# Kernel tuning notes

Measured on AMD Instinct MI355X. Metric: run time of the kernel, lower is better.

The kernel has to match this reference:

```python
import jax, jax.numpy as jnp
import numpy as np

D = 1024      # input_dim == memory_dim
HID = 1024    # hid_dim
NEG = 1e30


def setup_inputs() -> dict:
    key = jax.random.key(0)
    ks = jax.random.split(key, 9)
    N, LD, LM = 8, 2048, 512
    s = 1.0 / np.sqrt(D)
    return {
        "input": jax.random.normal(ks[0], (N, LD, D), jnp.float32),
        "memory": jax.random.normal(ks[1], (N, LM, D), jnp.float32),
        "mask": jnp.ones((N, LM), jnp.float32),
        # input_linear_1 / memory_linear_1: Linear(d, 1, bias=False)
        "in1_w": jax.random.normal(ks[2], (D,), jnp.float32) * s,
        "mem1_w": jax.random.normal(ks[3], (D,), jnp.float32) * s,
        # input_linear_2 / memory_linear_2: Linear(d, hid, bias=True), stored [d, hid]
        "in2_w": jax.random.normal(ks[4], (D, HID), jnp.float32) * s,
        "in2_b": jax.random.normal(ks[5], (HID,), jnp.float32) * s,
        "mem2_w": jax.random.normal(ks[6], (D, HID), jnp.float32) * s,
        "mem2_b": jax.random.normal(ks[7], (HID,), jnp.float32) * s,
    }


def reference(input, memory, mask, in1_w, mem1_w, in2_w, in2_b, mem2_w, mem2_b):
    # dropout=0.0 / eval mode -> identity
    dot_scale = jnp.asarray(np.sqrt(D), input.dtype)
    input_dot = jnp.einsum("nld,d->nl", input, in1_w)[:, :, None]      # [N,Ld,1]
    memory_dot = jnp.einsum("nmd,d->nm", memory, mem1_w)[:, None, :]   # [N,1,Lm]
    cross_dot = jnp.einsum("nld,nmd->nlm", input, memory) / dot_scale  # [N,Ld,Lm]
    att = input_dot + memory_dot + cross_dot
    att = att - NEG * (1.0 - mask[:, None, :])

    inp2 = jnp.einsum("nld,dh->nlh", input, in2_w) + in2_b    # [N,Ld,hid]
    mem2 = jnp.einsum("nmd,dh->nmh", memory, mem2_w) + mem2_b  # [N,Lm,hid]

    weight_one = jax.nn.softmax(att, axis=-1)                 # [N,Ld,Lm]
    output_one = jnp.einsum("nlm,nmh->nlh", weight_one, mem2)  # [N,Ld,hid]

    weight_two = jax.nn.softmax(jnp.max(att, axis=-1), axis=-1)  # [N,Ld]
    output_two = jnp.einsum("nl,nlh->nh", weight_two, inp2)[:, None, :]  # [N,1,hid]

    out = jnp.concatenate(
        [inp2, output_one, inp2 * output_one, output_two * output_one], axis=-1
    )  # [N,Ld,4*hid]
    return out, mem2
```

## Files before the change

kernel.cpp:

```cpp
#include <hip/hip_runtime.h>

typedef unsigned short u16;
typedef __attribute__((ext_vector_type(8))) short short8;
typedef __attribute__((ext_vector_type(4))) float f32x4;
typedef __attribute__((ext_vector_type(4))) unsigned short u16x4;

#define NSEQ 8
#define LD 2048
#define LM 512
#define DD 1024
#define HID 1024
#define M1 (NSEQ*LD)
#define M2 (NSEQ*LM)

#define GLOAD_LDS16(gp, lp) __builtin_amdgcn_global_load_lds( \
    (const __attribute__((address_space(1))) unsigned int*)(gp), \
    (__attribute__((address_space(3))) unsigned int*)(lp), 16, 0, 0)

__device__ __forceinline__ u16 f2bf(float f) {
    union { float f; unsigned int i; } v; v.f = f;
    unsigned int r = v.i + 0x7fffu + ((v.i >> 16) & 1u);
    return (u16)(r >> 16);
}
__device__ __forceinline__ float bf2f(u16 u) {
    union { unsigned int i; float f; } v; v.i = ((unsigned int)u) << 16; return v.f;
}

__global__ __launch_bounds__(256) void prep_rows2(
    const float* __restrict__ input, const float* __restrict__ memory,
    const float* __restrict__ in1_w, const float* __restrict__ mem1_w,
    const float* __restrict__ mask,
    u16* __restrict__ input_bf16, u16* __restrict__ memory_bf16,
    float* __restrict__ idot, float* __restrict__ mdotm) {
    const int row = blockIdx.x, t = threadIdx.x;
    const float* src; const float* w; u16* dst;
    if (row < M1) { src = input + (size_t)row * DD; w = in1_w;
                    dst = input_bf16 + (size_t)row * DD; }
    else { const int rm = row - M1; src = memory + (size_t)rm * DD; w = mem1_w;
           dst = memory_bf16 + (size_t)rm * DD; }
    f32x4 v = *(const f32x4*)(src + t * 4);
    f32x4 wv = *(const f32x4*)(w + t * 4);
    u16x4 o;
    #pragma unroll
    for (int i = 0; i < 4; i++) o[i] = f2bf(v[i]);
    *(u16x4*)(dst + t * 4) = o;
    float s = v[0]*wv[0] + v[1]*wv[1] + v[2]*wv[2] + v[3]*wv[3];
    #pragma unroll
    for (int off = 32; off; off >>= 1) s += __shfl_down(s, off);
    __shared__ float red[4];
    if ((t & 63) == 0) red[t >> 6] = s;
    __syncthreads();
    if (t == 0) {
        const float d = red[0] + red[1] + red[2] + red[3];
        if (row < M1) idot[row] = d;
        else { const int rm = row - M1;
               mdotm[rm] = d - 1e30f * (1.0f - mask[rm]); }
    }
}

__global__ void wtrans(const float* __restrict__ s0, const float* __restrict__ s1,
                       u16* __restrict__ d0, u16* __restrict__ d1) {
    __shared__ float tile[32][33];
    const float* src = blockIdx.z ? s1 : s0;
    u16* dst = blockIdx.z ? d1 : d0;
    const int c0 = blockIdx.x * 32, r0 = blockIdx.y * 32;
    const int tx = threadIdx.x, ty = threadIdx.y;
    #pragma unroll
    for (int yy = ty; yy < 32; yy += 8)
        tile[yy][tx] = src[(size_t)(r0 + yy) * DD + c0 + tx];
    __syncthreads();
    #pragma unroll
    for (int yy = ty; yy < 32; yy += 8)
        dst[(size_t)(c0 + yy) * DD + r0 + tx] = f2bf(tile[tx][yy]);
}

__global__ void transpose_f32_to_bf16(const float* __restrict__ src,
                                      u16* __restrict__ dst,
                                      int R, int C, size_t sn, size_t dn) {
    __shared__ float tile[32][33];
    src += (size_t)blockIdx.z * sn;
    dst += (size_t)blockIdx.z * dn;
    const int c0 = blockIdx.x * 32, r0 = blockIdx.y * 32;
    const int tx = threadIdx.x, ty = threadIdx.y;
    #pragma unroll
    for (int yy = ty; yy < 32; yy += 8)
        tile[yy][tx] = src[(size_t)(r0 + yy) * C + c0 + tx];
    __syncthreads();
    #pragma unroll
    for (int yy = ty; yy < 32; yy += 8)
        dst[(size_t)(c0 + yy) * R + r0 + tx] = f2bf(tile[tx][yy]);
}

template <int NT, int AI>
__global__ __launch_bounds__(512, 1) void gemmT(
    const u16* __restrict__ A, const u16* __restrict__ B,
    int lda, int ldb,
    float* __restrict__ out0, int ldc, const float* __restrict__ bias) {
    constexpr int BM = AI * 64;
    constexpr int BUFE = (BM + 128) * 64;
    __shared__ __align__(16) u16 lds[3 * BUFE];
    const int t = threadIdx.x;
    const int lane = t & 63, wave = t >> 6;
    const int wm = wave >> 2, wn = wave & 3;
    const int lr = lane & 15, kg = lane >> 4;
    const int bid = blockIdx.y * 8 + blockIdx.x;
    const int swz = (bid & 7) * gridDim.y + (bid >> 3);
    const int m0 = (swz >> 3) * BM, n0 = (swz & 7) * 128;

    const int srow = lane >> 3;
    const u16* gA[AI];
    const u16* gB[2];
    #pragma unroll
    for (int i = 0; i < AI; i++) {
        const int c = wave * AI + i;
        const int colb = ((lane & 7) * 16) ^ ((((c << 2) + (lane >> 4)) & 7) << 4);
        gA[i] = A + (size_t)(m0 + c * 8 + srow) * lda + (colb >> 1);
    }
    #pragma unroll
    for (int i = 0; i < 2; i++) {
        const int c = wave * 2 + i;
        const int colb = ((lane & 7) * 16) ^ ((((c << 2) + (lane >> 4)) & 7) << 4);
        gB[i] = B + (size_t)(n0 + c * 8 + srow) * ldb + (colb >> 1);
    }
    int offA[2 * AI], offB[2];
    #pragma unroll
    for (int i = 0; i < 2 * AI; i++) {
        const int row = wm * (BM / 2) + i * 16 + lr;
        offA[i] = (row * 128 + kg * 16) ^ (((row >> 1) & 7) << 4);
    }
    #pragma unroll
    for (int j = 0; j < 2; j++) {
        const int row = wn * 32 + j * 16 + lr;
        offB[j] = (BM * 64 * 2 + row * 128 + kg * 16) ^ (((row >> 1) & 7) << 4);
    }

    f32x4 acc[2 * AI][2];
    #pragma unroll
    for (int i = 0; i < 2 * AI; i++)
        #pragma unroll
        for (int j = 0; j < 2; j++) acc[i][j] = (f32x4){0.f, 0.f, 0.f, 0.f};

    #define STAGE(tt, buf) do {                                             \
        u16* la_ = &lds[(buf) * BUFE];                                      \
        u16* lb_ = la_ + BM * 64;                                           \
        const int ko_ = (tt) * 64;                                          \
        _Pragma("unroll")                                                   \
        for (int i_ = 0; i_ < AI; i_++)                                     \
            GLOAD_LDS16(gA[i_] + ko_, la_ + (wave * AI + i_) * 512);        \
        _Pragma("unroll")                                                   \
        for (int i_ = 0; i_ < 2; i_++)                                      \
            GLOAD_LDS16(gB[i_] + ko_, lb_ + (wave * 2 + i_) * 512);         \
    } while (0)
    #define WAITN() do {                                                    \
        if constexpr (AI == 4) asm volatile("s_waitcnt vmcnt(6)" ::: "memory"); \
        else                   asm volatile("s_waitcnt vmcnt(4)" ::: "memory"); \
    } while (0)

    STAGE(0, 0);
    STAGE(1, 1);
    WAITN();
    __builtin_amdgcn_s_barrier();
    __builtin_amdgcn_sched_barrier(0);

    int cb = 0, sb = 2;
    for (int tt = 0; tt < NT; ++tt) {
        if (tt + 2 < NT) STAGE(tt + 2, sb);
        __builtin_amdgcn_sched_barrier(0);
        const char* bb = (const char*)&lds[cb * BUFE];
        short8 bfr[2][2];
        #pragma unroll
        for (int j = 0; j < 2; j++)
            #pragma unroll
            for (int kh = 0; kh < 2; kh++)
                bfr[j][kh] = *(const short8*)(bb + (offB[j] ^ (kh * 64)));
        #pragma unroll
        for (int p = 0; p < AI; p++) {
            short8 af[2][2];
            #pragma unroll
            for (int q = 0; q < 2; q++)
                #pragma unroll
                for (int kh = 0; kh < 2; kh++)
                    af[q][kh] = *(const short8*)(bb + (offA[2 * p + q] ^ (kh * 64)));
            __builtin_amdgcn_s_setprio(1);
            #pragma unroll
            for (int q = 0; q < 2; q++)
                #pragma unroll
                for (int j = 0; j < 2; j++)
                    #pragma unroll
                    for (int kh = 0; kh < 2; kh++)
                        acc[2 * p + q][j] = __builtin_amdgcn_mfma_f32_16x16x32_bf16(
                            af[q][kh], bfr[j][kh], acc[2 * p + q][j], 0, 0, 0);
            __builtin_amdgcn_s_setprio(0);
        }
        if (tt + 2 < NT)      WAITN();
        else if (tt + 1 < NT) asm volatile("s_waitcnt vmcnt(0)" ::: "memory");
        __builtin_amdgcn_s_barrier();
        __builtin_amdgcn_sched_barrier(0);
        cb = (cb == 2) ? 0 : cb + 1;
        sb = (sb == 2) ? 0 : sb + 1;
    }
    #undef STAGE
    #undef WAITN

    #pragma unroll
    for (int i = 0; i < 2 * AI; i++) {
        #pragma unroll
        for (int j = 0; j < 2; j++) {
            const int col = n0 + wn * 32 + j * 16 + lr;
            #pragma unroll
            for (int r = 0; r < 4; r++) {
                const int row = m0 + wm * (BM / 2) + i * 16 + kg * 4 + r;
                out0[(size_t)row * ldc + col] = acc[i][j][r] + bias[col];
            }
        }
    }
}

__global__ __launch_bounds__(512, 2) void fused_gemm(
    const u16* __restrict__ A1, const u16* __restrict__ B1,
    const u16* __restrict__ A2, const u16* __restrict__ B2,
    float* __restrict__ out0,
    const float* __restrict__ bias, const float* __restrict__ ot) {
    constexpr int BUFE = (256 + 128) * 64;
    __shared__ __align__(16) u16 lds[3 * BUFE];
    const int t = threadIdx.x;
    const int lane = t & 63, wave = t >> 6;
    const int wm = wave >> 2, wn = wave & 3;
    const int lr = lane & 15, kg = lane >> 4;
    const int bid = blockIdx.y * 8 + blockIdx.x;
    const int swz = (bid & 7) * gridDim.y + (bid >> 3);
    const int m0 = (swz >> 3) * 256, n0 = (swz & 7) * 128;
    const int nb = m0 / LD;
    const u16* B2p = B2 + (size_t)nb * HID * LM;

    const int srow = lane >> 3;
    int colbA[4], colbB[2];
    const u16* gA[4];
    const u16* gB[2];
    #pragma unroll
    for (int i = 0; i < 4; i++) {
        const int c = wave * 4 + i;
        colbA[i] = ((lane & 7) * 16) ^ ((((c << 2) + (lane >> 4)) & 7) << 4);
        gA[i] = A1 + (size_t)(m0 + c * 8 + srow) * DD + (colbA[i] >> 1);
    }
    #pragma unroll
    for (int i = 0; i < 2; i++) {
        const int c = wave * 2 + i;
        colbB[i] = ((lane & 7) * 16) ^ ((((c << 2) + (lane >> 4)) & 7) << 4);
        gB[i] = B1 + (size_t)(n0 + c * 8 + srow) * DD + (colbB[i] >> 1);
    }
    int offA[8], offB[2];
    #pragma unroll
    for (int i = 0; i < 8; i++) {
        const int row = wm * 128 + i * 16 + lr;
        offA[i] = (row * 128 + kg * 16) ^ (((row >> 1) & 7) << 4);
    }
    #pragma unroll
    for (int j = 0; j < 2; j++) {
        const int row = wn * 32 + j * 16 + lr;
        offB[j] = (256 * 64 * 2 + row * 128 + kg * 16) ^ (((row >> 1) & 7) << 4);
    }

    #define STAGE(tt, buf) do {                                             \
        u16* la_ = &lds[(buf) * BUFE];                                      \
        u16* lb_ = la_ + 256 * 64;                                          \
        const int ko_ = (tt) * 64;                                          \
        _Pragma("unroll")                                                   \
        for (int i_ = 0; i_ < 4; i_++)                                      \
            GLOAD_LDS16(gA[i_] + ko_, la_ + (wave * 4 + i_) * 512);         \
        _Pragma("unroll")                                                   \
        for (int i_ = 0; i_ < 2; i_++)                                      \
            GLOAD_LDS16(gB[i_] + ko_, lb_ + (wave * 2 + i_) * 512);         \
    } while (0)

    #define KLOOP(NT, ACC)                                                  \
    do {                                                                    \
        STAGE(0, 0);                                                        \
        STAGE(1, 1);                                                        \
        asm volatile("s_waitcnt vmcnt(6)" ::: "memory");                    \
        __builtin_amdgcn_s_barrier();                                       \
        __builtin_amdgcn_sched_barrier(0);                                  \
        int cb = 0, sb = 2;                                                 \
        for (int tt = 0; tt < (NT); ++tt) {                                 \
            if (tt + 2 < (NT)) STAGE(tt + 2, sb);                           \
            __builtin_amdgcn_sched_barrier(0);                              \
            const char* bb = (const char*)&lds[cb * BUFE];                  \
            short8 bfr[2][2];                                               \
            _Pragma("unroll")                                               \
            for (int j = 0; j < 2; j++)                                     \
                _Pragma("unroll")                                           \
                for (int kh = 0; kh < 2; kh++)                              \
                    bfr[j][kh] = *(const short8*)(bb + (offB[j] ^ (kh * 64))); \
            _Pragma("unroll")                                               \
            for (int p = 0; p < 4; p++) {                                   \
                short8 af[2][2];                                            \
                _Pragma("unroll")                                           \
                for (int q = 0; q < 2; q++)                                 \
                    _Pragma("unroll")                                       \
                    for (int kh = 0; kh < 2; kh++)                          \
                        af[q][kh] = *(const short8*)(bb + (offA[2 * p + q] ^ (kh * 64))); \
                __builtin_amdgcn_s_setprio(1);                              \
                _Pragma("unroll")                                           \
                for (int q = 0; q < 2; q++)                                 \
                    _Pragma("unroll")                                       \
                    for (int j = 0; j < 2; j++)                             \
                        _Pragma("unroll")                                   \
                        for (int kh = 0; kh < 2; kh++)                      \
                            ACC[2 * p + q][j] = __builtin_amdgcn_mfma_f32_16x16x32_bf16( \
                                af[q][kh], bfr[j][kh], ACC[2 * p + q][j], 0, 0, 0); \
                __builtin_amdgcn_s_setprio(0);                              \
            }                                                               \
            if (tt + 2 < (NT))      asm volatile("s_waitcnt vmcnt(6)" ::: "memory"); \
            else if (tt + 1 < (NT)) asm volatile("s_waitcnt vmcnt(0)" ::: "memory"); \
            __builtin_amdgcn_s_barrier();                                   \
            __builtin_amdgcn_sched_barrier(0);                              \
            cb = (cb == 2) ? 0 : cb + 1;                                    \
            sb = (sb == 2) ? 0 : sb + 1;                                    \
        }                                                                   \
    } while (0)

    f32x4 acc1[8][2], acc2[8][2];
    #pragma unroll
    for (int i = 0; i < 8; i++)
        #pragma unroll
        for (int j = 0; j < 2; j++) {
            acc1[i][j] = (f32x4){0.f, 0.f, 0.f, 0.f};
            acc2[i][j] = (f32x4){0.f, 0.f, 0.f, 0.f};
        }

    KLOOP(16, acc1);

    #pragma unroll
    for (int i = 0; i < 4; i++) {
        const int c = wave * 4 + i;
        gA[i] = A2 + (size_t)(m0 + c * 8 + srow) * LM + (colbA[i] >> 1);
    }
    #pragma unroll
    for (int i = 0; i < 2; i++) {
        const int c = wave * 2 + i;
        gB[i] = B2p + (size_t)(n0 + c * 8 + srow) * LM + (colbB[i] >> 1);
    }

    KLOOP(8, acc2);

    #undef KLOOP
    #undef STAGE

    #pragma unroll
    for (int i = 0; i < 8; i++) {
        #pragma unroll
        for (int j = 0; j < 2; j++) {
            const int col = n0 + wn * 32 + j * 16 + lr;
            const float b = bias[col];
            const float otv = ot[nb * HID + col];
            #pragma unroll
            for (int r = 0; r < 4; r++) {
                const int row = m0 + wm * 128 + i * 16 + kg * 4 + r;
                const size_t o = (size_t)row * 4096 + col;
                const float i2 = acc1[i][j][r] + b;
                const float o1 = acc2[i][j][r];
                out0[o] = i2;
                out0[o + 1024] = o1;
                out0[o + 2048] = i2 * o1;
                out0[o + 3072] = otv * o1;
            }
        }
    }
}

__global__ __launch_bounds__(512, 1) void att_softmax(
    const u16* __restrict__ A, const u16* __restrict__ B,
    const float* __restrict__ idot, const float* __restrict__ mdotm,
    u16* __restrict__ P, float* __restrict__ rowmax) {
    constexpr int ABUF = 64 * 64;
    constexpr int BBUF = 256 * 64;
    constexpr int BUFE = ABUF + BBUF;
    __shared__ __align__(16) u16 lds[3 * BUFE];
    const int t = threadIdx.x, lane = t & 63, wave = t >> 6;
    const int wm = wave >> 2, wn = wave & 3;
    const int lr = lane & 15, kg = lane >> 4;
    const int bid = blockIdx.x;
    const int swz = (bid & 7) * 32 + (bid >> 3);
    const int m0 = swz * 64;
    const int nb = m0 >> 11;
    const u16* Bp = B + (size_t)nb * LM * DD;

    const int srow = lane >> 3;
    const u16* gA;
    {
        const int colb = ((lane & 7) * 16) ^ ((((wave << 2) + (lane >> 4)) & 7) << 4);
        gA = A + (size_t)(m0 + wave * 8 + srow) * DD + (colb >> 1);
    }
    const u16* gB[4];
    #pragma unroll
    for (int i = 0; i < 4; i++) {
        const int c = wave * 4 + i;
        const int colb = ((lane & 7) * 16) ^ ((((c << 2) + (lane >> 4)) & 7) << 4);
        gB[i] = Bp + (size_t)(c * 8 + srow) * DD + (colb >> 1);
    }
    int offA[2], offB[4];
    #pragma unroll
    for (int i = 0; i < 2; i++) {
        const int row = wm * 32 + i * 16 + lr;
        offA[i] = (row * 128 + kg * 16) ^ (((row >> 1) & 7) << 4);
    }
    #pragma unroll
    for (int j = 0; j < 4; j++) {
        const int row = wn * 64 + j * 16 + lr;
        offB[j] = (ABUF * 2 + row * 128 + kg * 16) ^ (((row >> 1) & 7) << 4);
    }

    f32x4 acc[2][8];
    #pragma unroll
    for (int i = 0; i < 2; i++)
        #pragma unroll
        for (int j = 0; j < 8; j++) acc[i][j] = (f32x4){0.f, 0.f, 0.f, 0.f};

    #define ASTAGE(tt, buf, pofs) do {                                      \
        u16* la_ = &lds[(buf) * BUFE];                                      \
        u16* lb_ = la_ + ABUF;                                              \
        const int ko_ = (tt) * 64;                                          \
        GLOAD_LDS16(gA + ko_, la_ + wave * 512);                            \
        _Pragma("unroll")                                                   \
        for (int i_ = 0; i_ < 4; i_++)                                      \
            GLOAD_LDS16(gB[i_] + (pofs) + ko_, lb_ + (wave * 4 + i_) * 512); \
    } while (0)

    for (int c = 0; c < 2; c++) {
        const size_t pofs = (size_t)c * 256 * DD;
        ASTAGE(0, 0, pofs);
        ASTAGE(1, 1, pofs);
        asm volatile("s_waitcnt vmcnt(5)" ::: "memory");
        __builtin_amdgcn_s_barrier();
        __builtin_amdgcn_sched_barrier(0);
        int cb = 0, sb = 2;
        for (int tt = 0; tt < 16; ++tt) {
            if (tt + 2 < 16) ASTAGE(tt + 2, sb, pofs);
            __builtin_amdgcn_sched_barrier(0);
            const char* bb = (const char*)&lds[cb * BUFE];
            short8 af[2][2];
            #pragma unroll
            for (int i = 0; i < 2; i++)
                #pragma unroll
                for (int kh = 0; kh < 2; kh++)
                    af[i][kh] = *(const short8*)(bb + (offA[i] ^ (kh * 64)));
            #pragma unroll
            for (int j = 0; j < 4; j++) {
                short8 bf[2];
                #pragma unroll
                for (int kh = 0; kh < 2; kh++)
                    bf[kh] = *(const short8*)(bb + (offB[j] ^ (kh * 64)));
                __builtin_amdgcn_s_setprio(1);
                #pragma unroll
                for (int i = 0; i < 2; i++)
                    #pragma unroll
                    for (int kh = 0; kh < 2; kh++)
                        acc[i][c * 4 + j] = __builtin_amdgcn_mfma_f32_16x16x32_bf16(
                            af[i][kh], bf[kh], acc[i][c * 4 + j], 0, 0, 0);
                __builtin_amdgcn_s_setprio(0);
            }
            if (tt + 2 < 16)      asm volatile("s_waitcnt vmcnt(5)" ::: "memory");
            else if (tt + 1 < 16) asm volatile("s_waitcnt vmcnt(0)" ::: "memory");
            __builtin_amdgcn_s_barrier();
            __builtin_amdgcn_sched_barrier(0);
            cb = (cb == 2) ? 0 : cb + 1;
            sb = (sb == 2) ? 0 : sb + 1;
        }
    }
    #undef ASTAGE

    float* redm = (float*)lds;
    float* reds = redm + 256;
    float mdv[8];
    #pragma unroll
    for (int cj = 0; cj < 8; cj++)
        mdv[cj] = mdotm[nb * LM + (cj >> 2) * 256 + wn * 64 + (cj & 3) * 16 + lr];
    float idv[8];
    #pragma unroll
    for (int i = 0; i < 2; i++)
        #pragma unroll
        for (int r = 0; r < 4; r++)
            idv[i * 4 + r] = idot[m0 + wm * 32 + i * 16 + kg * 4 + r];
    float pm[8];
    #pragma unroll
    for (int i = 0; i < 2; i++)
        #pragma unroll
        for (int r = 0; r < 4; r++) {
            float mx = -3.0e38f;
            #pragma unroll
            for (int cj = 0; cj < 8; cj++) {
                const float v = acc[i][cj][r] * 0.03125f + idv[i * 4 + r] + mdv[cj];
                acc[i][cj][r] = v;
                mx = fmaxf(mx, v);
            }
            pm[i * 4 + r] = mx;
        }
    #pragma unroll
    for (int w = 1; w < 16; w <<= 1)
        #pragma unroll
        for (int q = 0; q < 8; q++) pm[q] = fmaxf(pm[q], __shfl_xor(pm[q], w));
    if (lr == 0) {
        #pragma unroll
        for (int i = 0; i < 2; i++)
            #pragma unroll
            for (int r = 0; r < 4; r++)
                redm[(wm * 32 + i * 16 + kg * 4 + r) * 4 + wn] = pm[i * 4 + r];
    }
    __syncthreads();
    float Mr[8], ps[8];
    #pragma unroll
    for (int i = 0; i < 2; i++)
        #pragma unroll
        for (int r = 0; r < 4; r++) {
            const int row = wm * 32 + i * 16 + kg * 4 + r;
            const float a = fmaxf(redm[row * 4 + 0], redm[row * 4 + 1]);
            const float b = fmaxf(redm[row * 4 + 2], redm[row * 4 + 3]);
            Mr[i * 4 + r] = fmaxf(a, b);
            float s = 0.f;
            #pragma unroll
            for (int cj = 0; cj < 8; cj++) {
                const float e = __expf(acc[i][cj][r] - Mr[i * 4 + r]);
                acc[i][cj][r] = e;
                s += e;
            }
            ps[i * 4 + r] = s;
        }
    #pragma unroll
    for (int w = 1; w < 16; w <<= 1)
        #pragma unroll
        for (int q = 0; q < 8; q++) ps[q] += __shfl_xor(ps[q], w);
    if (lr == 0) {
        #pragma unroll
        for (int i = 0; i < 2; i++)
            #pragma unroll
            for (int r = 0; r < 4; r++)
                reds[(wm * 32 + i * 16 + kg * 4 + r) * 4 + wn] = ps[i * 4 + r];
    }
    __syncthreads();
    #pragma unroll
    for (int i = 0; i < 2; i++)
        #pragma unroll
        for (int r = 0; r < 4; r++) {
            const int row = wm * 32 + i * 16 + kg * 4 + r;
            const float inv = 1.0f / (reds[row * 4 + 0] + reds[row * 4 + 1] +
                                      reds[row * 4 + 2] + reds[row * 4 + 3]);
            if (wn == 0 && lr == 0) rowmax[m0 + row] = Mr[i * 4 + r];
            #pragma unroll
            for (int cj = 0; cj < 8; cj++)
                P[(size_t)(m0 + row) * LM +
                  (cj >> 2) * 256 + wn * 64 + (cj & 3) * 16 + lr] =
                    f2bf(acc[i][cj][r] * inv);
        }
}

__global__ __launch_bounds__(256) void xbar_partial(
    const float* __restrict__ rowmax, const u16* __restrict__ X,
    float* __restrict__ part) {
    const int lz = blockIdx.x, n = blockIdx.y, t = threadIdx.x;
    const float* rm = rowmax + (size_t)n * LD;
    float v[8];
    float m = -3.0e38f;
    #pragma unroll
    for (int i = 0; i < 8; i++) { v[i] = rm[t + i * 256]; m = fmaxf(m, v[i]); }
    #pragma unroll
    for (int off = 32; off; off >>= 1) m = fmaxf(m, __shfl_down(m, off));
    __shared__ float sm[4], ss[4];
    __shared__ float wl[64];
    if ((t & 63) == 0) sm[t >> 6] = m;
    __syncthreads();
    const float M = fmaxf(fmaxf(sm[0], sm[1]), fmaxf(sm[2], sm[3]));
    float s = 0.f;
    #pragma unroll
    for (int i = 0; i < 8; i++) s += __expf(v[i] - M);
    #pragma unroll
    for (int off = 32; off; off >>= 1) s += __shfl_down(s, off);
    if ((t & 63) == 0) ss[t >> 6] = s;
    __syncthreads();
    const float invS = 1.0f / (ss[0] + ss[1] + ss[2] + ss[3]);
    if (t < 64) wl[t] = __expf(rm[lz * 64 + t] - M) * invS;
    __syncthreads();
    const u16* xp = X + ((size_t)n * LD + lz * 64) * DD + t * 4;
    f32x4 acc = {0.f, 0.f, 0.f, 0.f};
    #pragma unroll 4
    for (int l = 0; l < 64; l++) {
        u16x4 x = *(const u16x4*)(xp + (size_t)l * DD);
        const float w = wl[l];
        acc[0] += w * bf2f(x[0]); acc[1] += w * bf2f(x[1]);
        acc[2] += w * bf2f(x[2]); acc[3] += w * bf2f(x[3]);
    }
    *(f32x4*)&part[((size_t)n * 32 + lz) * HID + t * 4] = acc;
}

__global__ __launch_bounds__(256) void ot_final2(
    const float* __restrict__ part, const u16* __restrict__ Wt,
    const float* __restrict__ bias, float* __restrict__ ot) {
    const int hc = blockIdx.x, n = blockIdx.y, t = threadIdx.x;
    __shared__ float xb[HID];
    f32x4 s = {0.f, 0.f, 0.f, 0.f};
    #pragma unroll
    for (int i = 0; i < 32; i++) {
        f32x4 p = *(const f32x4*)&part[((size_t)n * 32 + i) * HID + t * 4];
        s[0] += p[0]; s[1] += p[1]; s[2] += p[2]; s[3] += p[3];
    }
    *(f32x4*)&xb[t * 4] = s;
    __syncthreads();
    const int h = hc * 128 + (t >> 1);
    const int d0 = (t & 1) * 512;
    float a = 0.f;
    #pragma unroll 4
    for (int d = 0; d < 512; d += 8) {
        short8 w8 = *(const short8*)&Wt[(size_t)h * DD + d0 + d];
        #pragma unroll
        for (int j = 0; j < 8; j++) a += bf2f((u16)w8[j]) * xb[d0 + d + j];
    }
    a += __shfl_xor(a, 1);
    if ((t & 1) == 0) ot[(size_t)n * HID + h] = a + bias[h];
}

extern "C" void kernel_launch(void* const* d_in, const int* in_sizes, int n_in,
                              void* d_out, int out_size, void* d_ws, size_t ws_size,
                              hipStream_t stream) {
    const float* input  = (const float*)d_in[0];
    const float* memory = (const float*)d_in[1];
    const float* mask   = (const float*)d_in[2];
    const float* in1_w  = (const float*)d_in[3];
    const float* mem1_w = (const float*)d_in[4];
    const float* in2_w  = (const float*)d_in[5];
    const float* in2_b  = (const float*)d_in[6];
    const float* mem2_w = (const float*)d_in[7];
    const float* mem2_b = (const float*)d_in[8];

    float* out = (float*)d_out;
    float* outTail = out + (size_t)M1 * 4096;

    char* ws = (char*)d_ws;
    size_t off = 0;
    auto alloc = [&](size_t bytes) -> void* {
        void* p = ws + off;
        off = (off + bytes + 255) & ~(size_t)255;
        return p;
    };
    u16* input_bf16  = (u16*)alloc((size_t)M1 * DD * 2);
    u16* memory_bf16 = (u16*)alloc((size_t)M2 * DD * 2);
    u16* in2_wt      = (u16*)alloc((size_t)HID * DD * 2);
    u16* mem2_wt     = (u16*)alloc((size_t)HID * DD * 2);
    u16* mem2t       = (u16*)alloc((size_t)NSEQ * HID * LM * 2);
    u16* P           = (u16*)alloc((size_t)M1 * LM * 2);
    float* idot      = (float*)alloc((size_t)M1 * 4);
    float* mdotm     = (float*)alloc((size_t)M2 * 4);
    float* rowmax    = (float*)alloc((size_t)M1 * 4);
    float* ot        = (float*)alloc((size_t)NSEQ * HID * 4);
    float* part      = (float*)alloc((size_t)NSEQ * 32 * HID * 4);

    prep_rows2<<<M1 + M2, 256, 0, stream>>>(input, memory, in1_w, mem1_w, mask,
                                            input_bf16, memory_bf16, idot, mdotm);
    wtrans<<<dim3(32, 32, 2), dim3(32, 8), 0, stream>>>(in2_w, mem2_w, in2_wt, mem2_wt);
    gemmT<16, 2><<<dim3(8, M2 / 128), 512, 0, stream>>>(
        memory_bf16, mem2_wt, DD, DD, outTail, HID, mem2_b);
    transpose_f32_to_bf16<<<dim3(HID / 32, LM / 32, NSEQ), dim3(32, 8), 0, stream>>>(
        outTail, mem2t, LM, HID, (size_t)LM * HID, (size_t)HID * LM);
    att_softmax<<<M1 / 64, 512, 0, stream>>>(
        input_bf16, memory_bf16, idot, mdotm, P, rowmax);
    xbar_partial<<<dim3(32, NSEQ), 256, 0, stream>>>(rowmax, input_bf16, part);
    ot_final2<<<dim3(8, NSEQ), 256, 0, stream>>>(part, in2_wt, in2_b, ot);
    fused_gemm<<<dim3(8, M1 / 256), 512, 0, stream>>>(
        input_bf16, in2_wt, P, mem2t, out, in2_b, ot);
}
```

Measured before the change: 203.4 us.

## Fuse prep kernels, emit transposed mem2 from GEMM epilogue, interleave output stores

Merges the row-prep and weight-transpose kernels into one launch, and has the mem2 GEMM write its bf16 transposed copy through LDS in its epilogue, which removes the separate transpose kernel and its re-read of mem2. In the fused output GEMM the P·mem2 loop now runs first. The output_one stores are spread across iterations of the second K-loop, so they overlap with MFMA work, and the vmcnt waits are adjusted to account for them. This cuts launches and global traffic but adds LDS epilogue work and riskier hand-tuned wait counts.

```diff
diff --git a/kernel.cpp b/kernel.cpp
--- a/kernel.cpp
+++ b/kernel.cpp
@@ -26,77 +26,63 @@
     union { unsigned int i; float f; } v; v.i = ((unsigned int)u) << 16; return v.f;
 }
 
-__global__ __launch_bounds__(256) void prep_rows2(
+__global__ __launch_bounds__(256) void prep_all(
     const float* __restrict__ input, const float* __restrict__ memory,
     const float* __restrict__ in1_w, const float* __restrict__ mem1_w,
     const float* __restrict__ mask,
+    const float* __restrict__ in2_w, const float* __restrict__ mem2_w,
     u16* __restrict__ input_bf16, u16* __restrict__ memory_bf16,
+    u16* __restrict__ in2_wt, u16* __restrict__ mem2_wt,
     float* __restrict__ idot, float* __restrict__ mdotm) {
-    const int row = blockIdx.x, t = threadIdx.x;
-    const float* src; const float* w; u16* dst;
-    if (row < M1) { src = input + (size_t)row * DD; w = in1_w;
-                    dst = input_bf16 + (size_t)row * DD; }
-    else { const int rm = row - M1; src = memory + (size_t)rm * DD; w = mem1_w;
-           dst = memory_bf16 + (size_t)rm * DD; }
-    f32x4 v = *(const f32x4*)(src + t * 4);
-    f32x4 wv = *(const f32x4*)(w + t * 4);
-    u16x4 o;
-    #pragma unroll
-    for (int i = 0; i < 4; i++) o[i] = f2bf(v[i]);
-    *(u16x4*)(dst + t * 4) = o;
-    float s = v[0]*wv[0] + v[1]*wv[1] + v[2]*wv[2] + v[3]*wv[3];
-    #pragma unroll
-    for (int off = 32; off; off >>= 1) s += __shfl_down(s, off);
-    __shared__ float red[4];
-    if ((t & 63) == 0) red[t >> 6] = s;
-    __syncthreads();
-    if (t == 0) {
-        const float d = red[0] + red[1] + red[2] + red[3];
-        if (row < M1) idot[row] = d;
-        else { const int rm = row - M1;
-               mdotm[rm] = d - 1e30f * (1.0f - mask[rm]); }
-    }
-}
-
-__global__ void wtrans(const float* __restrict__ s0, const float* __restrict__ s1,
-                       u16* __restrict__ d0, u16* __restrict__ d1) {
     __shared__ float tile[32][33];
-    const float* src = blockIdx.z ? s1 : s0;
-    u16* dst = blockIdx.z ? d1 : d0;
-    const int c0 = blockIdx.x * 32, r0 = blockIdx.y * 32;
-    const int tx = threadIdx.x, ty = threadIdx.y;
-    #pragma unroll
-    for (int yy = ty; yy < 32; yy += 8)
-        tile[yy][tx] = src[(size_t)(r0 + yy) * DD + c0 + tx];
-    __syncthreads();
-    #pragma unroll
-    for (int yy = ty; yy < 32; yy += 8)
-        dst[(size_t)(c0 + yy) * DD + r0 + tx] = f2bf(tile[tx][yy]);
-}
-
-__global__ void transpose_f32_to_bf16(const float* __restrict__ src,
-                                      u16* __restrict__ dst,
-                                      int R, int C, size_t sn, size_t dn) {
-    __shared__ float tile[32][33];
-    src += (size_t)blockIdx.z * sn;
-    dst += (size_t)blockIdx.z * dn;
-    const int c0 = blockIdx.x * 32, r0 = blockIdx.y * 32;
-    const int tx = threadIdx.x, ty = threadIdx.y;
-    #pragma unroll
-    for (int yy = ty; yy < 32; yy += 8)
-        tile[yy][tx] = src[(size_t)(r0 + yy) * C + c0 + tx];
-    __syncthreads();
-    #pragma unroll
-    for (int yy = ty; yy < 32; yy += 8)
-        dst[(size_t)(c0 + yy) * R + r0 + tx] = f2bf(tile[tx][yy]);
-}
-
-template <int NT, int AI>
-__global__ __launch_bounds__(512, 1) void gemmT(
+    const int b = blockIdx.x, t = threadIdx.x;
+    if (b < M1 + M2) {
+        const float* src; const float* w; u16* dst;
+        if (b < M1) { src = input + (size_t)b * DD; w = in1_w;
+                      dst = input_bf16 + (size_t)b * DD; }
+        else { const int rm = b - M1; src = memory + (size_t)rm * DD; w = mem1_w;
+               dst = memory_bf16 + (size_t)rm * DD; }
+        f32x4 v = *(const f32x4*)(src + t * 4);
+        f32x4 wv = *(const f32x4*)(w + t * 4);
+        u16x4 o;
+        #pragma unroll
+        for (int i = 0; i < 4; i++) o[i] = f2bf(v[i]);
+        *(u16x4*)(dst + t * 4) = o;
+        float s = v[0]*wv[0] + v[1]*wv[1] + v[2]*wv[2] + v[3]*wv[3];
+        #pragma unroll
+        for (int off = 32; off; off >>= 1) s += __shfl_down(s, off);
+        if ((t & 63) == 0) tile[0][t >> 6] = s;
+        __syncthreads();
+        if (t == 0) {
+            const float d = tile[0][0] + tile[0][1] + tile[0][2] + tile[0][3];
+            if (b < M1) idot[b] = d;
+            else { const int rm = b - M1;
+                   mdotm[rm] = d - 1e30f * (1.0f - mask[rm]); }
+        }
+    } else {
+        const int wb = b - (M1 + M2);
+        const int z = wb >> 10;
+        const int tid = wb & 1023;
+        const int c0 = (tid & 31) * 32, r0 = (tid >> 5) * 32;
+        const float* src = z ? mem2_w : in2_w;
+        u16* dst = z ? mem2_wt : in2_wt;
+        const int tx = t & 31, ty = t >> 5;
+        #pragma unroll
+        for (int yy = ty; yy < 32; yy += 8)
+            tile[yy][tx] = src[(size_t)(r0 + yy) * DD + c0 + tx];
+        __syncthreads();
+        #pragma unroll
+        for (int yy = ty; yy < 32; yy += 8)
+            dst[(size_t)(c0 + yy) * DD + r0 + tx] = f2bf(tile[tx][yy]);
+    }
+}
+
+template <int NT>
+__global__ __launch_bounds__(512, 1) void gemm_mem2(
     const u16* __restrict__ A, const u16* __restrict__ B,
-    int lda, int ldb,
-    float* __restrict__ out0, int ldc, const float* __restrict__ bias) {
-    constexpr int BM = AI * 64;
+    float* __restrict__ out0, const float* __restrict__ bias,
+    u16* __restrict__ mem2t) {
+    constexpr int AI = 2, BM = 128;
     constexpr int BUFE = (BM + 128) * 64;
     __shared__ __align__(16) u16 lds[3 * BUFE];
     const int t = threadIdx.x;
@@ -114,13 +100,13 @@
     for (int i = 0; i < AI; i++) {
         const int c = wave * AI + i;
         const int colb = ((lane & 7) * 16) ^ ((((c << 2) + (lane >> 4)) & 7) << 4);
-        gA[i] = A + (size_t)(m0 + c * 8 + srow) * lda + (colb >> 1);
+        gA[i] = A + (size_t)(m0 + c * 8 + srow) * DD + (colb >> 1);
     }
     #pragma unroll
     for (int i = 0; i < 2; i++) {
         const int c = wave * 2 + i;
         const int colb = ((lane & 7) * 16) ^ ((((c << 2) + (lane >> 4)) & 7) << 4);
-        gB[i] = B + (size_t)(n0 + c * 8 + srow) * ldb + (colb >> 1);
+        gB[i] = B + (size_t)(n0 + c * 8 + srow) * DD + (colb >> 1);
     }
     int offA[2 * AI], offB[2];
     #pragma unroll
@@ -151,14 +137,10 @@
         for (int i_ = 0; i_ < 2; i_++)                                      \
             GLOAD_LDS16(gB[i_] + ko_, lb_ + (wave * 2 + i_) * 512);         \
     } while (0)
-    #define WAITN() do {                                                    \
-        if constexpr (AI == 4) asm volatile("s_waitcnt vmcnt(6)" ::: "memory"); \
-        else                   asm volatile("s_waitcnt vmcnt(4)" ::: "memory"); \
-    } while (0)
 
     STAGE(0, 0);
     STAGE(1, 1);
-    WAITN();
+    asm volatile("s_waitcnt vmcnt(4)" ::: "memory");
     __builtin_amdgcn_s_barrier();
     __builtin_amdgcn_sched_barrier(0);
 
@@ -192,7 +174,7 @@
                             af[q][kh], bfr[j][kh], acc[2 * p + q][j], 0, 0, 0);
             __builtin_amdgcn_s_setprio(0);
         }
-        if (tt + 2 < NT)      WAITN();
+        if (tt + 2 < NT)      asm volatile("s_waitcnt vmcnt(4)" ::: "memory");
         else if (tt + 1 < NT) asm volatile("s_waitcnt vmcnt(0)" ::: "memory");
         __builtin_amdgcn_s_barrier();
         __builtin_amdgcn_sched_barrier(0);
@@ -200,19 +182,31 @@
         sb = (sb == 2) ? 0 : sb + 1;
     }
     #undef STAGE
-    #undef WAITN
-
+
+    u16* ldsT = (u16*)lds;
     #pragma unroll
     for (int i = 0; i < 2 * AI; i++) {
         #pragma unroll
         for (int j = 0; j < 2; j++) {
-            const int col = n0 + wn * 32 + j * 16 + lr;
+            const int lcol = wn * 32 + j * 16 + lr;
+            const float bv = bias[n0 + lcol];
             #pragma unroll
             for (int r = 0; r < 4; r++) {
-                const int row = m0 + wm * (BM / 2) + i * 16 + kg * 4 + r;
-                out0[(size_t)row * ldc + col] = acc[i][j][r] + bias[col];
+                const int lrow = wm * (BM / 2) + i * 16 + kg * 4 + r;
+                const float v = acc[i][j][r] + bv;
+                out0[(size_t)(m0 + lrow) * HID + n0 + lcol] = v;
+                ldsT[lcol * 136 + lrow] = f2bf(v);
             }
         }
+    }
+    __syncthreads();
+    const int nb = m0 >> 9, mloc = m0 & 511;
+    #pragma unroll
+    for (int s = 0; s < 4; s++) {
+        const int idx = s * 512 + t;
+        const int hrow = idx >> 4, seg = idx & 15;
+        short8 v8 = *(const short8*)&ldsT[hrow * 136 + seg * 8];
+        *(short8*)&mem2t[((size_t)nb * HID + n0 + hrow) * LM + mloc + seg * 8] = v8;
     }
 }
 
@@ -241,13 +235,13 @@
     for (int i = 0; i < 4; i++) {
         const int c = wave * 4 + i;
         colbA[i] = ((lane & 7) * 16) ^ ((((c << 2) + (lane >> 4)) & 7) << 4);
-        gA[i] = A1 + (size_t)(m0 + c * 8 + srow) * DD + (colbA[i] >> 1);
+        gA[i] = A2 + (size_t)(m0 + c * 8 + srow) * LM + (colbA[i] >> 1);
     }
     #pragma unroll
     for (int i = 0; i < 2; i++) {
         const int c = wave * 2 + i;
         colbB[i] = ((lane & 7) * 16) ^ ((((c << 2) + (lane >> 4)) & 7) << 4);
-        gB[i] = B1 + (size_t)(n0 + c * 8 + srow) * DD + (colbB[i] >> 1);
+        gB[i] = B2p + (size_t)(n0 + c * 8 + srow) * LM + (colbB[i] >> 1);
     }
     int offA[8], offB[2];
     #pragma unroll
@@ -273,52 +267,6 @@
             GLOAD_LDS16(gB[i_] + ko_, lb_ + (wave * 2 + i_) * 512);         \
     } while (0)
 
-    #define KLOOP(NT, ACC)                                                  \
-    do {                                                                    \
-        STAGE(0, 0);                                                        \
-        STAGE(1, 1);                                                        \
-        asm volatile("s_waitcnt vmcnt(6)" ::: "memory");                    \
-        __builtin_amdgcn_s_barrier();                                       \
-        __builtin_amdgcn_sched_barrier(0);                                  \
-        int cb = 0, sb = 2;                                                 \
-        for (int tt = 0; tt < (NT); ++tt) {                                 \
-            if (tt + 2 < (NT)) STAGE(tt + 2, sb);                           \
-            __builtin_amdgcn_sched_barrier(0);                              \
-            const char* bb = (const char*)&lds[cb * BUFE];                  \
-            short8 bfr[2][2];                                               \
-            _Pragma("unroll")                                               \
-            for (int j = 0; j < 2; j++)                                     \
-                _Pragma("unroll")                                           \
-                for (int kh = 0; kh < 2; kh++)                              \
-                    bfr[j][kh] = *(const short8*)(bb + (offB[j] ^ (kh * 64))); \
-            _Pragma("unroll")                                               \
-            for (int p = 0; p < 4; p++) {                                   \
-                short8 af[2][2];                                            \
-                _Pragma("unroll")                                           \
-                for (int q = 0; q < 2; q++)                                 \
-                    _Pragma("unroll")                                       \
-                    for (int kh = 0; kh < 2; kh++)                          \
-                        af[q][kh] = *(const short8*)(bb + (offA[2 * p + q] ^ (kh * 64))); \
-                __builtin_amdgcn_s_setprio(1);                              \
-                _Pragma("unroll")                                           \
-                for (int q = 0; q < 2; q++)                                 \
-                    _Pragma("unroll")                                       \
-                    for (int j = 0; j < 2; j++)                             \
-                        _Pragma("unroll")                                   \
-                        for (int kh = 0; kh < 2; kh++)                      \
-                            ACC[2 * p + q][j] = __builtin_amdgcn_mfma_f32_16x16x32_bf16( \
-                                af[q][kh], bfr[j][kh], ACC[2 * p + q][j], 0, 0, 0); \
-                __builtin_amdgcn_s_setprio(0);                              \
-            }                                                               \
-            if (tt + 2 < (NT))      asm volatile("s_waitcnt vmcnt(6)" ::: "memory"); \
-            else if (tt + 1 < (NT)) asm volatile("s_waitcnt vmcnt(0)" ::: "memory"); \
-            __builtin_amdgcn_s_barrier();                                   \
-            __builtin_amdgcn_sched_barrier(0);                              \
-            cb = (cb == 2) ? 0 : cb + 1;                                    \
-            sb = (sb == 2) ? 0 : sb + 1;                                    \
-        }                                                                   \
-    } while (0)
-
     f32x4 acc1[8][2], acc2[8][2];
     #pragma unroll
     for (int i = 0; i < 8; i++)
@@ -328,22 +276,117 @@
             acc2[i][j] = (f32x4){0.f, 0.f, 0.f, 0.f};
         }
 
-    KLOOP(16, acc1);
+    {
+        STAGE(0, 0);
+        STAGE(1, 1);
+        asm volatile("s_waitcnt vmcnt(6)" ::: "memory");
+        __builtin_amdgcn_s_barrier();
+        __builtin_amdgcn_sched_barrier(0);
+        int cb = 0, sb = 2;
+        for (int tt = 0; tt < 8; ++tt) {
+            if (tt + 2 < 8) STAGE(tt + 2, sb);
+            __builtin_amdgcn_sched_barrier(0);
+            const char* bb = (const char*)&lds[cb * BUFE];
+            short8 bfr[2][2];
+            #pragma unroll
+            for (int j = 0; j < 2; j++)
+                #pragma unroll
+                for (int kh = 0; kh < 2; kh++)
+                    bfr[j][kh] = *(const short8*)(bb + (offB[j] ^ (kh * 64)));
+            #pragma unroll
+            for (int p = 0; p < 4; p++) {
+                short8 af[2][2];
+                #pragma unroll
+                for (int q = 0; q < 2; q++)
+                    #pragma unroll
+                    for (int kh = 0; kh < 2; kh++)
+                        af[q][kh] = *(const short8*)(bb + (offA[2 * p + q] ^ (kh * 64)));
+                __builtin_amdgcn_s_setprio(1);
+                #pragma unroll
+                for (int q = 0; q < 2; q++)
+                    #pragma unroll
+                    for (int j = 0; j < 2; j++)
+                        #pragma unroll
+                        for (int kh = 0; kh < 2; kh++)
+                            acc2[2 * p + q][j] = __builtin_amdgcn_mfma_f32_16x16x32_bf16(
+                                af[q][kh], bfr[j][kh], acc2[2 * p + q][j], 0, 0, 0);
+                __builtin_amdgcn_s_setprio(0);
+            }
+            if (tt + 2 < 8)      asm volatile("s_waitcnt vmcnt(6)" ::: "memory");
+            else if (tt + 1 < 8) asm volatile("s_waitcnt vmcnt(0)" ::: "memory");
+            __builtin_amdgcn_s_barrier();
+            __builtin_amdgcn_sched_barrier(0);
+            cb = (cb == 2) ? 0 : cb + 1;
+            sb = (sb == 2) ? 0 : sb + 1;
+        }
+    }
 
     #pragma unroll
     for (int i = 0; i < 4; i++) {
         const int c = wave * 4 + i;
-        gA[i] = A2 + (size_t)(m0 + c * 8 + srow) * LM + (colbA[i] >> 1);
+        gA[i] = A1 + (size_t)(m0 + c * 8 + srow) * DD + (colbA[i] >> 1);
     }
     #pragma unroll
     for (int i = 0; i < 2; i++) {
         const int c = wave * 2 + i;
-        gB[i] = B2p + (size_t)(n0 + c * 8 + srow) * LM + (colbB[i] >> 1);
-    }
-
-    KLOOP(8, acc2);
-
-    #undef KLOOP
+        gB[i] = B1 + (size_t)(n0 + c * 8 + srow) * DD + (colbB[i] >> 1);
+    }
+
+    {
+        STAGE(0, 0);
+        STAGE(1, 1);
+        asm volatile("s_waitcnt vmcnt(6)" ::: "memory");
+        __builtin_amdgcn_s_barrier();
+        __builtin_amdgcn_sched_barrier(0);
+        int cb = 0, sb = 2;
+        #pragma unroll
+        for (int tt = 0; tt < 16; ++tt) {
+            if (tt + 2 < 16) STAGE(tt + 2, sb);
+            __builtin_amdgcn_sched_barrier(0);
+            const char* bb = (const char*)&lds[cb * BUFE];
+            short8 bfr[2][2];
+            #pragma unroll
+            for (int j = 0; j < 2; j++)
+                #pragma unroll
+                for (int kh = 0; kh < 2; kh++)
+                    bfr[j][kh] = *(const short8*)(bb + (offB[j] ^ (kh * 64)));
+            #pragma unroll
+            for (int p = 0; p < 4; p++) {
+                short8 af[2][2];
+                #pragma unroll
+                for (int q = 0; q < 2; q++)
+                    #pragma unroll
+                    for (int kh = 0; kh < 2; kh++)
+                        af[q][kh] = *(const short8*)(bb + (offA[2 * p + q] ^ (kh * 64)));
+                __builtin_amdgcn_s_setprio(1);
+                #pragma unroll
+                for (int q = 0; q < 2; q++)
+                    #pragma unroll
+                    for (int j = 0; j < 2; j++)
+                        #pragma unroll
+                        for (int kh = 0; kh < 2; kh++)
+                            acc1[2 * p + q][j] = __builtin_amdgcn_mfma_f32_16x16x32_bf16(
+                                af[q][kh], bfr[j][kh], acc1[2 * p + q][j], 0, 0, 0);
+                __builtin_amdgcn_s_setprio(0);
+            }
+            {
+                const int di = tt >> 1, dj = tt & 1;
+                const int col = n0 + wn * 32 + dj * 16 + lr;
+                #pragma unroll
+                for (int r = 0; r < 4; r++) {
+                    const int row = m0 + wm * 128 + di * 16 + kg * 4 + r;
+                    out0[(size_t)row * 4096 + 1024 + col] = acc2[di][dj][r];
+                }
+            }
+            if (tt == 0)           asm volatile("s_waitcnt vmcnt(10)" ::: "memory");
+            else if (tt + 2 < 16)  asm volatile("s_waitcnt vmcnt(14)" ::: "memory");
+            else if (tt == 14)     asm volatile("s_waitcnt vmcnt(8)" ::: "memory");
+            __builtin_amdgcn_s_barrier();
+            __builtin_amdgcn_sched_barrier(0);
+            cb = (cb == 2) ? 0 : cb + 1;
+            sb = (sb == 2) ? 0 : sb + 1;
+        }
+    }
     #undef STAGE
 
     #pragma unroll
@@ -360,7 +403,6 @@
                 const float i2 = acc1[i][j][r] + b;
                 const float o1 = acc2[i][j][r];
                 out0[o] = i2;
-                out0[o + 1024] = o1;
                 out0[o + 2048] = i2 * o1;
                 out0[o + 3072] = otv * o1;
             }
@@ -652,13 +694,11 @@
     float* ot        = (float*)alloc((size_t)NSEQ * HID * 4);
     float* part      = (float*)alloc((size_t)NSEQ * 32 * HID * 4);
 
-    prep_rows2<<<M1 + M2, 256, 0, stream>>>(input, memory, in1_w, mem1_w, mask,
-                                            input_bf16, memory_bf16, idot, mdotm);
-    wtrans<<<dim3(32, 32, 2), dim3(32, 8), 0, stream>>>(in2_w, mem2_w, in2_wt, mem2_wt);
-    gemmT<16, 2><<<dim3(8, M2 / 128), 512, 0, stream>>>(
-        memory_bf16, mem2_wt, DD, DD, outTail, HID, mem2_b);
-    transpose_f32_to_bf16<<<dim3(HID / 32, LM / 32, NSEQ), dim3(32, 8), 0, stream>>>(
-        outTail, mem2t, LM, HID, (size_t)LM * HID, (size_t)HID * LM);
+    prep_all<<<M1 + M2 + 2048, 256, 0, stream>>>(
+        input, memory, in1_w, mem1_w, mask, in2_w, mem2_w,
+        input_bf16, memory_bf16, in2_wt, mem2_wt, idot, mdotm);
+    gemm_mem2<16><<<dim3(8, M2 / 128), 512, 0, stream>>>(
+        memory_bf16, mem2_wt, outTail, mem2_b, mem2t);
     att_softmax<<<M1 / 64, 512, 0, stream>>>(
         input_bf16, memory_bf16, idot, mdotm, P, rowmax);
     xbar_partial<<<dim3(32, NSEQ), 256, 0, stream>>>(rowmax, input_bf16, part);
```

New measurement: 218.6 us. 7.5% more time.

## Merge weight transpose into prep kernel and fuse mem2 transpose into GEMM epilogue

Applied to the files above, without the earlier changes.

The weight transpose kernel is folded into the row-prep kernel as extra blocks, so one launch does both. The mem2 GEMM epilogue now also writes a transposed bf16 copy through LDS, which removes the separate transpose kernel and its re-read of the fp32 mem2 output. This saves two launches and some global traffic, at the cost of extra LDS staging and a barrier in the GEMM epilogue.

```diff
diff --git a/kernel.cpp b/kernel.cpp
--- a/kernel.cpp
+++ b/kernel.cpp
@@ -26,77 +26,63 @@
     union { unsigned int i; float f; } v; v.i = ((unsigned int)u) << 16; return v.f;
 }
 
-__global__ __launch_bounds__(256) void prep_rows2(
+__global__ __launch_bounds__(256) void prep_all(
     const float* __restrict__ input, const float* __restrict__ memory,
     const float* __restrict__ in1_w, const float* __restrict__ mem1_w,
     const float* __restrict__ mask,
+    const float* __restrict__ in2_w, const float* __restrict__ mem2_w,
     u16* __restrict__ input_bf16, u16* __restrict__ memory_bf16,
+    u16* __restrict__ in2_wt, u16* __restrict__ mem2_wt,
     float* __restrict__ idot, float* __restrict__ mdotm) {
-    const int row = blockIdx.x, t = threadIdx.x;
-    const float* src; const float* w; u16* dst;
-    if (row < M1) { src = input + (size_t)row * DD; w = in1_w;
-                    dst = input_bf16 + (size_t)row * DD; }
-    else { const int rm = row - M1; src = memory + (size_t)rm * DD; w = mem1_w;
-           dst = memory_bf16 + (size_t)rm * DD; }
-    f32x4 v = *(const f32x4*)(src + t * 4);
-    f32x4 wv = *(const f32x4*)(w + t * 4);
-    u16x4 o;
-    #pragma unroll
-    for (int i = 0; i < 4; i++) o[i] = f2bf(v[i]);
-    *(u16x4*)(dst + t * 4) = o;
-    float s = v[0]*wv[0] + v[1]*wv[1] + v[2]*wv[2] + v[3]*wv[3];
-    #pragma unroll
-    for (int off = 32; off; off >>= 1) s += __shfl_down(s, off);
-    __shared__ float red[4];
-    if ((t & 63) == 0) red[t >> 6] = s;
-    __syncthreads();
-    if (t == 0) {
-        const float d = red[0] + red[1] + red[2] + red[3];
-        if (row < M1) idot[row] = d;
-        else { const int rm = row - M1;
-               mdotm[rm] = d - 1e30f * (1.0f - mask[rm]); }
-    }
-}
-
-__global__ void wtrans(const float* __restrict__ s0, const float* __restrict__ s1,
-                       u16* __restrict__ d0, u16* __restrict__ d1) {
     __shared__ float tile[32][33];
-    const float* src = blockIdx.z ? s1 : s0;
-    u16* dst = blockIdx.z ? d1 : d0;
-    const int c0 = blockIdx.x * 32, r0 = blockIdx.y * 32;
-    const int tx = threadIdx.x, ty = threadIdx.y;
-    #pragma unroll
-    for (int yy = ty; yy < 32; yy += 8)
-        tile[yy][tx] = src[(size_t)(r0 + yy) * DD + c0 + tx];
-    __syncthreads();
-    #pragma unroll
-    for (int yy = ty; yy < 32; yy += 8)
-        dst[(size_t)(c0 + yy) * DD + r0 + tx] = f2bf(tile[tx][yy]);
-}
-
-__global__ void transpose_f32_to_bf16(const float* __restrict__ src,
-                                      u16* __restrict__ dst,
-                                      int R, int C, size_t sn, size_t dn) {
-    __shared__ float tile[32][33];
-    src += (size_t)blockIdx.z * sn;
-    dst += (size_t)blockIdx.z * dn;
-    const int c0 = blockIdx.x * 32, r0 = blockIdx.y * 32;
-    const int tx = threadIdx.x, ty = threadIdx.y;
-    #pragma unroll
-    for (int yy = ty; yy < 32; yy += 8)
-        tile[yy][tx] = src[(size_t)(r0 + yy) * C + c0 + tx];
-    __syncthreads();
-    #pragma unroll
-    for (int yy = ty; yy < 32; yy += 8)
-        dst[(size_t)(c0 + yy) * R + r0 + tx] = f2bf(tile[tx][yy]);
-}
-
-template <int NT, int AI>
-__global__ __launch_bounds__(512, 1) void gemmT(
+    const int b = blockIdx.x, t = threadIdx.x;
+    if (b < M1 + M2) {
+        const float* src; const float* w; u16* dst;
+        if (b < M1) { src = input + (size_t)b * DD; w = in1_w;
+                      dst = input_bf16 + (size_t)b * DD; }
+        else { const int rm = b - M1; src = memory + (size_t)rm * DD; w = mem1_w;
+               dst = memory_bf16 + (size_t)rm * DD; }
+        f32x4 v = *(const f32x4*)(src + t * 4);
+        f32x4 wv = *(const f32x4*)(w + t * 4);
+        u16x4 o;
+        #pragma unroll
+        for (int i = 0; i < 4; i++) o[i] = f2bf(v[i]);
+        *(u16x4*)(dst + t * 4) = o;
+        float s = v[0]*wv[0] + v[1]*wv[1] + v[2]*wv[2] + v[3]*wv[3];
+        #pragma unroll
+        for (int off = 32; off; off >>= 1) s += __shfl_down(s, off);
+        if ((t & 63) == 0) tile[0][t >> 6] = s;
+        __syncthreads();
+        if (t == 0) {
+            const float d = tile[0][0] + tile[0][1] + tile[0][2] + tile[0][3];
+            if (b < M1) idot[b] = d;
+            else { const int rm = b - M1;
+                   mdotm[rm] = d - 1e30f * (1.0f - mask[rm]); }
+        }
+    } else {
+        const int wb = b - (M1 + M2);
+        const int z = wb >> 10;
+        const int tid = wb & 1023;
+        const int c0 = (tid & 31) * 32, r0 = (tid >> 5) * 32;
+        const float* src = z ? mem2_w : in2_w;
+        u16* dst = z ? mem2_wt : in2_wt;
+        const int tx = t & 31, ty = t >> 5;
+        #pragma unroll
+        for (int yy = ty; yy < 32; yy += 8)
+            tile[yy][tx] = src[(size_t)(r0 + yy) * DD + c0 + tx];
+        __syncthreads();
+        #pragma unroll
+        for (int yy = ty; yy < 32; yy += 8)
+            dst[(size_t)(c0 + yy) * DD + r0 + tx] = f2bf(tile[tx][yy]);
+    }
+}
+
+template <int NT>
+__global__ __launch_bounds__(512, 1) void gemm_mem2(
     const u16* __restrict__ A, const u16* __restrict__ B,
-    int lda, int ldb,
-    float* __restrict__ out0, int ldc, const float* __restrict__ bias) {
-    constexpr int BM = AI * 64;
+    float* __restrict__ out0, const float* __restrict__ bias,
+    u16* __restrict__ mem2t) {
+    constexpr int AI = 2, BM = 128;
     constexpr int BUFE = (BM + 128) * 64;
     __shared__ __align__(16) u16 lds[3 * BUFE];
     const int t = threadIdx.x;
@@ -114,13 +100,13 @@
     for (int i = 0; i < AI; i++) {
         const int c = wave * AI + i;
         const int colb = ((lane & 7) * 16) ^ ((((c << 2) + (lane >> 4)) & 7) << 4);
-        gA[i] = A + (size_t)(m0 + c * 8 + srow) * lda + (colb >> 1);
+        gA[i] = A + (size_t)(m0 + c * 8 + srow) * DD + (colb >> 1);
     }
     #pragma unroll
     for (int i = 0; i < 2; i++) {
         const int c = wave * 2 + i;
         const int colb = ((lane & 7) * 16) ^ ((((c << 2) + (lane >> 4)) & 7) << 4);
-        gB[i] = B + (size_t)(n0 + c * 8 + srow) * ldb + (colb >> 1);
+        gB[i] = B + (size_t)(n0 + c * 8 + srow) * DD + (colb >> 1);
     }
     int offA[2 * AI], offB[2];
     #pragma unroll
@@ -151,14 +137,10 @@
         for (int i_ = 0; i_ < 2; i_++)                                      \
             GLOAD_LDS16(gB[i_] + ko_, lb_ + (wave * 2 + i_) * 512);         \
     } while (0)
-    #define WAITN() do {                                                    \
-        if constexpr (AI == 4) asm volatile("s_waitcnt vmcnt(6)" ::: "memory"); \
-        else                   asm volatile("s_waitcnt vmcnt(4)" ::: "memory"); \
-    } while (0)
 
     STAGE(0, 0);
     STAGE(1, 1);
-    WAITN();
+    asm volatile("s_waitcnt vmcnt(4)" ::: "memory");
     __builtin_amdgcn_s_barrier();
     __builtin_amdgcn_sched_barrier(0);
 
@@ -192,7 +174,7 @@
                             af[q][kh], bfr[j][kh], acc[2 * p + q][j], 0, 0, 0);
             __builtin_amdgcn_s_setprio(0);
         }
-        if (tt + 2 < NT)      WAITN();
+        if (tt + 2 < NT)      asm volatile("s_waitcnt vmcnt(4)" ::: "memory");
         else if (tt + 1 < NT) asm volatile("s_waitcnt vmcnt(0)" ::: "memory");
         __builtin_amdgcn_s_barrier();
         __builtin_amdgcn_sched_barrier(0);
@@ -200,19 +182,31 @@
         sb = (sb == 2) ? 0 : sb + 1;
     }
     #undef STAGE
-    #undef WAITN
-
+
+    u16* ldsT = (u16*)lds;
     #pragma unroll
     for (int i = 0; i < 2 * AI; i++) {
         #pragma unroll
         for (int j = 0; j < 2; j++) {
-            const int col = n0 + wn * 32 + j * 16 + lr;
+            const int lcol = wn * 32 + j * 16 + lr;
+            const float bv = bias[n0 + lcol];
             #pragma unroll
             for (int r = 0; r < 4; r++) {
-                const int row = m0 + wm * (BM / 2) + i * 16 + kg * 4 + r;
-                out0[(size_t)row * ldc + col] = acc[i][j][r] + bias[col];
+                const int lrow = wm * (BM / 2) + i * 16 + kg * 4 + r;
+                const float v = acc[i][j][r] + bv;
+                out0[(size_t)(m0 + lrow) * HID + n0 + lcol] = v;
+                ldsT[lcol * 136 + lrow] = f2bf(v);
             }
         }
+    }
+    __syncthreads();
+    const int nb = m0 >> 9, mloc = m0 & 511;
+    #pragma unroll
+    for (int s = 0; s < 4; s++) {
+        const int idx = s * 512 + t;
+        const int hrow = idx >> 4, seg = idx & 15;
+        short8 v8 = *(const short8*)&ldsT[hrow * 136 + seg * 8];
+        *(short8*)&mem2t[((size_t)nb * HID + n0 + hrow) * LM + mloc + seg * 8] = v8;
     }
 }
 
@@ -652,13 +646,11 @@
     float* ot        = (float*)alloc((size_t)NSEQ * HID * 4);
     float* part      = (float*)alloc((size_t)NSEQ * 32 * HID * 4);
 
-    prep_rows2<<<M1 + M2, 256, 0, stream>>>(input, memory, in1_w, mem1_w, mask,
-                                            input_bf16, memory_bf16, idot, mdotm);
-    wtrans<<<dim3(32, 32, 2), dim3(32, 8), 0, stream>>>(in2_w, mem2_w, in2_wt, mem2_wt);
-    gemmT<16, 2><<<dim3(8, M2 / 128), 512, 0, stream>>>(
-        memory_bf16, mem2_wt, DD, DD, outTail, HID, mem2_b);
-    transpose_f32_to_bf16<<<dim3(HID / 32, LM / 32, NSEQ), dim3(32, 8), 0, stream>>>(
-        outTail, mem2t, LM, HID, (size_t)LM * HID, (size_t)HID * LM);
+    prep_all<<<M1 + M2 + 2048, 256, 0, stream>>>(
+        input, memory, in1_w, mem1_w, mask, in2_w, mem2_w,
+        input_bf16, memory_bf16, in2_wt, mem2_wt, idot, mdotm);
+    gemm_mem2<16><<<dim3(8, M2 / 128), 512, 0, stream>>>(
+        memory_bf16, mem2_wt, outTail, mem2_b, mem2t);
     att_softmax<<<M1 / 64, 512, 0, stream>>>(
         input_bf16, memory_bf16, idot, mdotm, P, rowmax);
     xbar_partial<<<dim3(32, NSEQ), 256, 0, stream>>>(rowmax, input_bf16, part);
```

After: 196.8 us. 3.3% less time.
